# Performance work log

Hardware: AMD Instinct MI355X
Metric: run time of the kernel (lower is better)

## Reference

```python
import jax, jax.numpy as jnp
import numpy as np

N_ATOMS, N_EDGES, N_TRIPLES = 5000, 200000, 4000000
D_NODE, D_EDGE, N_BASIS = 128, 128, 9


def setup_inputs() -> dict:
    key = jax.random.key(0)
    ks = jax.random.split(key, 14)
    inp = {
        "node_feat": jax.random.normal(ks[0], (N_ATOMS, D_NODE), jnp.float32),
        "edge_feat": jax.random.normal(ks[1], (N_EDGES, D_EDGE), jnp.float32),
        "three_basis": jax.random.normal(ks[2], (N_TRIPLES, N_BASIS), jnp.float32),
        "three_cutoff": jax.random.uniform(ks[3], (N_EDGES,), jnp.float32),
        # learned params: update_network_atom = Linear(d_node->n_basis) + sigmoid
        "W_atom": jax.random.normal(ks[4], (D_NODE, N_BASIS), jnp.float32) / np.sqrt(D_NODE).astype(np.float32),
        "b_atom": jnp.zeros((N_BASIS,), jnp.float32),
        # update_network_bond = gated MLP: silu(Linear) * sigmoid(Linear), n_basis->d_edge
        "W_gate": jax.random.normal(ks[5], (N_BASIS, D_EDGE), jnp.float32) / np.sqrt(N_BASIS).astype(np.float32),
        "b_gate": jnp.zeros((D_EDGE,), jnp.float32),
        "W_sig": jax.random.normal(ks[6], (N_BASIS, D_EDGE), jnp.float32) / np.sqrt(N_BASIS).astype(np.float32),
        "b_sig": jnp.zeros((D_EDGE,), jnp.float32),
        # graph structure (int constants)
        "graph_dst": jax.random.randint(ks[7], (N_EDGES,), 0, N_ATOMS, jnp.int32),
        "lg_src": jax.random.randint(ks[8], (N_TRIPLES,), 0, N_EDGES, jnp.int32),
        "lg_dst": jax.random.randint(ks[9], (N_TRIPLES,), 0, N_EDGES, jnp.int32),
        # sorted segment ids == get_segment_indices_from_n(n_triple_ij)
        "segment_ids": jnp.sort(jax.random.randint(ks[10], (N_TRIPLES,), 0, N_EDGES, jnp.int32)),
    }
    return inp


def reference(node_feat, edge_feat, three_basis, three_cutoff,
              W_atom, b_atom, W_gate, b_gate, W_sig, b_sig,
              graph_dst, lg_src, lg_dst, segment_ids):
    # Eq.2: transform node features, gather end atom of each triple's second bond
    atoms = jax.nn.sigmoid(node_feat @ W_atom + b_atom)          # [n_atoms, n_basis]
    end_atom_index = graph_dst[lg_dst]                           # [n_triples]
    basis = three_basis * atoms[end_atom_index]                  # [n_triples, n_basis]
    # cutoff weights per triple (dead code in the provided source: scatter uses basis)
    weights = three_cutoff[lg_src] * three_cutoff[lg_dst]        # [n_triples]
    _ = basis * weights[:, None]
    # scatter-sum triples back to their bond
    new_bonds = jax.ops.segment_sum(basis, segment_ids, num_segments=N_EDGES)  # [n_edges, n_basis]
    # Eq.3: gated MLP bond update
    update = jax.nn.silu(new_bonds @ W_gate + b_gate) * jax.nn.sigmoid(new_bonds @ W_sig + b_sig)
    return edge_feat + update
```

## Files before the change

### kernel.cpp

```cpp
#include <hip/hip_runtime.h>

#define D_NODE    128
#define N_BASIS   9
#define AH_STRIDE 16
#define D_EDGE    128

#define BLOCK_C 256
#define TPT     4
#define CHUNK   (BLOCK_C * TPT)
#define SEG_CAP 512

typedef _Float16 half8 __attribute__((ext_vector_type(8)));

__device__ __forceinline__ float fast_sigmoid(float x) {
    return __builtin_amdgcn_rcpf(1.0f + __expf(-x));
}

__global__ __launch_bounds__(256) void atoms_kernel(
    const float* __restrict__ node_feat,
    const float* __restrict__ W_atom,
    const float* __restrict__ b_atom,
    _Float16* __restrict__ atoms, int n_atoms)
{
    __shared__ float sW[D_NODE * N_BASIS];
    for (int t = threadIdx.x; t < D_NODE * N_BASIS; t += 256)
        sW[t] = W_atom[t];
    __syncthreads();
    int idx = blockIdx.x * 256 + threadIdx.x;
    int total = n_atoms * N_BASIS;
    if (idx >= total) return;
    int a = idx / N_BASIS;
    int b = idx - a * N_BASIS;
    const float* row = node_feat + a * D_NODE;
    float acc = b_atom[b];
#pragma unroll 8
    for (int i = 0; i < D_NODE; ++i)
        acc += row[i] * sW[i * N_BASIS + b];
    atoms[a * AH_STRIDE + b] = (_Float16)fast_sigmoid(acc);
}

__global__ __launch_bounds__(256) void edge_atoms_kernel(
    const _Float16* __restrict__ atoms,
    const int* __restrict__ graph_dst,
    _Float16* __restrict__ ea, int n_edges)
{
    int e = blockIdx.x * 256 + threadIdx.x;
    if (e >= n_edges) return;
    int a = graph_dst[e];
    const _Float16* ap = atoms + (size_t)a * AH_STRIDE;
    half8 h = *(const half8*)ap;
    _Float16 h8 = ap[8];
    _Float16* dp = ea + (size_t)e * AH_STRIDE;
    *(half8*)dp = h;
    dp[8] = h8;
}

#define FLUSH_RUN()                                                          \
    do {                                                                     \
        if (use_lds) {                                                       \
            float* dst_ = lacc + (cur - seg_first) * N_BASIS;                \
            _Pragma("unroll")                                                \
            for (int k_ = 0; k_ < N_BASIS; ++k_)                             \
                atomicAdd(&dst_[k_], sum[k_]);                               \
        } else {                                                             \
            float* dst_ = new_bonds + (size_t)cur * N_BASIS;                 \
            _Pragma("unroll")                                                \
            for (int k_ = 0; k_ < N_BASIS; ++k_)                             \
                unsafeAtomicAdd(&dst_[k_], sum[k_]);                         \
        }                                                                    \
    } while (0)

template<bool EA>
__global__ __launch_bounds__(BLOCK_C) void triple_kernel(
    const float* __restrict__ three_basis,
    const _Float16* __restrict__ atab,
    const int*   __restrict__ graph_dst,
    const int*   __restrict__ lg_dst,
    const int*   __restrict__ seg,
    float* __restrict__ new_bonds,
    int n_triples)
{
    __shared__ float lacc[SEG_CAP * N_BASIS];
    __shared__ int sh_first, sh_last;

    const int tid = threadIdx.x;
    const int chunk_start = blockIdx.x * CHUNK;
    const int t0 = chunk_start + tid * TPT;

    if (tid == 0) sh_first = seg[chunk_start];
    if (tid == BLOCK_C - 1) {
        int last = chunk_start + CHUNK;
        if (last > n_triples) last = n_triples;
        sh_last = seg[last - 1];
    }
    for (int i = tid; i < SEG_CAP * N_BASIS; i += BLOCK_C)
        lacc[i] = 0.0f;
    __syncthreads();

    const int seg_first = sh_first;
    const int range = sh_last - seg_first + 1;
    const bool use_lds = (range <= SEG_CAP);

    if (t0 + TPT <= n_triples) {
        float tb[TPT * N_BASIS];
        const float4* tb4 = (const float4*)(three_basis + (size_t)t0 * N_BASIS);
#pragma unroll
        for (int q = 0; q < 9; ++q)
            *(float4*)&tb[q * 4] = tb4[q];

        const int4 sg4 = *(const int4*)(seg + t0);
        const int4 ld4 = *(const int4*)(lg_dst + t0);
        int sgs[TPT] = { sg4.x, sg4.y, sg4.z, sg4.w };

        int ridx[TPT];
        if (EA) {
            ridx[0] = ld4.x; ridx[1] = ld4.y; ridx[2] = ld4.z; ridx[3] = ld4.w;
        } else {
            ridx[0] = graph_dst[ld4.x];
            ridx[1] = graph_dst[ld4.y];
            ridx[2] = graph_dst[ld4.z];
            ridx[3] = graph_dst[ld4.w];
        }
        half8 hh[TPT];
        _Float16 h8[TPT];
#pragma unroll
        for (int i = 0; i < TPT; ++i) {
            const _Float16* ap = atab + (size_t)ridx[i] * AH_STRIDE;
            hh[i] = *(const half8*)ap;
            h8[i] = ap[8];
        }

        float sum[N_BASIS];
        int cur = sgs[0];
#pragma unroll
        for (int k = 0; k < N_BASIS; ++k) sum[k] = 0.0f;

#pragma unroll
        for (int i = 0; i < TPT; ++i) {
            if (sgs[i] != cur) {
                FLUSH_RUN();
                cur = sgs[i];
#pragma unroll
                for (int k = 0; k < N_BASIS; ++k) sum[k] = 0.0f;
            }
#pragma unroll
            for (int k = 0; k < 8; ++k)
                sum[k] += tb[i * N_BASIS + k] * (float)hh[i][k];
            sum[8] += tb[i * N_BASIS + 8] * (float)h8[i];
        }
        FLUSH_RUN();
    } else if (t0 < n_triples) {
        for (int t = t0; t < n_triples; ++t) {
            int cur = seg[t];
            int r = EA ? lg_dst[t] : graph_dst[lg_dst[t]];
            const float* tbr = three_basis + (size_t)t * N_BASIS;
            const _Float16* ar = atab + (size_t)r * AH_STRIDE;
            float sum[N_BASIS];
#pragma unroll
            for (int k = 0; k < N_BASIS; ++k) sum[k] = tbr[k] * (float)ar[k];
            FLUSH_RUN();
        }
    }

    __syncthreads();

    if (use_lds) {
        int total = range * N_BASIS;
        for (int idx = tid; idx < total; idx += BLOCK_C) {
            int r = idx / N_BASIS;
            int k = idx - r * N_BASIS;
            float v = lacc[idx];
            int s = seg_first + r;
            if (r == 0 || r == range - 1) {
                if (v != 0.0f)
                    unsafeAtomicAdd(&new_bonds[(size_t)s * N_BASIS + k], v);
            } else {
                new_bonds[(size_t)s * N_BASIS + k] = v;
            }
        }
    }
}

__global__ __launch_bounds__(256) void mlp_kernel(
    const float* __restrict__ edge_feat,
    const float* __restrict__ new_bonds,
    const float* __restrict__ W_gate, const float* __restrict__ b_gate,
    const float* __restrict__ W_sig,  const float* __restrict__ b_sig,
    float* __restrict__ out, int n_edges)
{
    const int tid  = threadIdx.x;
    const int grp  = tid >> 5;
    const int c    = (tid & 31) * 4;
    const int e0   = (blockIdx.x * 8 + grp) * 4;
    if (e0 >= n_edges) return;
    const int nvalid = (n_edges - e0) < 4 ? (n_edges - e0) : 4;

    float nb[4][N_BASIS];
#pragma unroll
    for (int j = 0; j < 4; ++j) {
        const float* nbr = new_bonds + (size_t)(e0 + (j < nvalid ? j : 0)) * N_BASIS;
#pragma unroll
        for (int k = 0; k < N_BASIS; ++k) nb[j][k] = nbr[k];
    }

    float4 bg = *(const float4*)(b_gate + c);
    float4 bs = *(const float4*)(b_sig + c);
    float4 g[4], s[4];
#pragma unroll
    for (int j = 0; j < 4; ++j) { g[j] = bg; s[j] = bs; }

#pragma unroll
    for (int k = 0; k < N_BASIS; ++k) {
        float4 wg = *(const float4*)(W_gate + k * D_EDGE + c);
        float4 ws = *(const float4*)(W_sig  + k * D_EDGE + c);
#pragma unroll
        for (int j = 0; j < 4; ++j) {
            g[j].x += nb[j][k] * wg.x; g[j].y += nb[j][k] * wg.y;
            g[j].z += nb[j][k] * wg.z; g[j].w += nb[j][k] * wg.w;
            s[j].x += nb[j][k] * ws.x; s[j].y += nb[j][k] * ws.y;
            s[j].z += nb[j][k] * ws.z; s[j].w += nb[j][k] * ws.w;
        }
    }

#pragma unroll
    for (int j = 0; j < 4; ++j) {
        if (j < nvalid) {
            int e = e0 + j;
            float4 ef = *(const float4*)(edge_feat + (size_t)e * D_EDGE + c);
            float4 o;
            o.x = ef.x + g[j].x * fast_sigmoid(g[j].x) * fast_sigmoid(s[j].x);
            o.y = ef.y + g[j].y * fast_sigmoid(g[j].y) * fast_sigmoid(s[j].y);
            o.z = ef.z + g[j].z * fast_sigmoid(g[j].z) * fast_sigmoid(s[j].z);
            o.w = ef.w + g[j].w * fast_sigmoid(g[j].w) * fast_sigmoid(s[j].w);
            *(float4*)(out + (size_t)e * D_EDGE + c) = o;
        }
    }
}

extern "C" void kernel_launch(void* const* d_in, const int* in_sizes, int n_in,
                              void* d_out, int out_size, void* d_ws, size_t ws_size,
                              hipStream_t stream) {
    const float* node_feat   = (const float*)d_in[0];
    const float* edge_feat   = (const float*)d_in[1];
    const float* three_basis = (const float*)d_in[2];
    const float* W_atom      = (const float*)d_in[4];
    const float* b_atom      = (const float*)d_in[5];
    const float* W_gate      = (const float*)d_in[6];
    const float* b_gate      = (const float*)d_in[7];
    const float* W_sig       = (const float*)d_in[8];
    const float* b_sig       = (const float*)d_in[9];
    const int*   graph_dst   = (const int*)d_in[10];
    const int*   lg_dst      = (const int*)d_in[12];
    const int*   seg         = (const int*)d_in[13];

    int n_atoms   = in_sizes[0] / D_NODE;
    int n_edges   = in_sizes[1] / D_EDGE;
    int n_triples = in_sizes[2] / N_BASIS;

    size_t atoms_bytes = ((size_t)n_atoms * AH_STRIDE * sizeof(_Float16) + 255) & ~(size_t)255;
    size_t ea_bytes    = ((size_t)n_edges * AH_STRIDE * sizeof(_Float16) + 255) & ~(size_t)255;
    size_t nb_bytes    = (size_t)n_edges * N_BASIS * sizeof(float);

    bool use_ea = (ws_size >= atoms_bytes + ea_bytes + nb_bytes);

    _Float16* atoms = (_Float16*)d_ws;
    _Float16* ea    = (_Float16*)((char*)d_ws + atoms_bytes);
    float* new_bonds = (float*)((char*)d_ws + atoms_bytes + (use_ea ? ea_bytes : 0));

    hipMemsetAsync(new_bonds, 0, nb_bytes, stream);

    atoms_kernel<<<(n_atoms * N_BASIS + 255) / 256, 256, 0, stream>>>(
        node_feat, W_atom, b_atom, atoms, n_atoms);

    if (use_ea) {
        edge_atoms_kernel<<<(n_edges + 255) / 256, 256, 0, stream>>>(
            atoms, graph_dst, ea, n_edges);
        triple_kernel<true><<<(n_triples + CHUNK - 1) / CHUNK, BLOCK_C, 0, stream>>>(
            three_basis, ea, graph_dst, lg_dst, seg, new_bonds, n_triples);
    } else {
        triple_kernel<false><<<(n_triples + CHUNK - 1) / CHUNK, BLOCK_C, 0, stream>>>(
            three_basis, atoms, graph_dst, lg_dst, seg, new_bonds, n_triples);
    }

    mlp_kernel<<<(n_edges + 31) / 32, 256, 0, stream>>>(
        edge_feat, new_bonds, W_gate, b_gate, W_sig, b_sig, (float*)d_out, n_edges);
}
```

Before: 420.5 us.

## Stage triple basis via global_load_lds, split atom table, drop edge-atom kernel

Each wave of the triple kernel now bulk-copies its slab of three_basis into LDS with the async global_load_lds path and then reads it back, replacing strided per-thread float4 loads. The padded 16-half atom table is split into an 8-half array plus a separate scalar array. The edge-atom precompute kernel is removed, so the triple kernel always does the graph_dst indirection. The MLP kernel stages weights and new_bonds rows in shared memory, and SEG_CAP is halved, which trades more global-atomic fallbacks for lower LDS usage.

```diff
diff --git a/kernel.cpp b/kernel.cpp
--- a/kernel.cpp
+++ b/kernel.cpp
@@ -1,16 +1,20 @@
 #include <hip/hip_runtime.h>
 
-#define D_NODE    128
-#define N_BASIS   9
-#define AH_STRIDE 16
-#define D_EDGE    128
+#define D_NODE   128
+#define N_BASIS  9
+#define D_EDGE   128
 
 #define BLOCK_C 256
 #define TPT     4
 #define CHUNK   (BLOCK_C * TPT)
-#define SEG_CAP 512
+#define WAVE_T  (64 * TPT)
+#define SLAB_F  (WAVE_T * N_BASIS)
+#define SEG_CAP 256
 
 typedef _Float16 half8 __attribute__((ext_vector_type(8)));
+
+#define AS1(p) ((const __attribute__((address_space(1))) void*)(p))
+#define AS3(p) ((__attribute__((address_space(3))) void*)(p))
 
 __device__ __forceinline__ float fast_sigmoid(float x) {
     return __builtin_amdgcn_rcpf(1.0f + __expf(-x));
@@ -20,7 +24,8 @@
     const float* __restrict__ node_feat,
     const float* __restrict__ W_atom,
     const float* __restrict__ b_atom,
-    _Float16* __restrict__ atoms, int n_atoms)
+    _Float16* __restrict__ atoms8,
+    _Float16* __restrict__ atoms1, int n_atoms)
 {
     __shared__ float sW[D_NODE * N_BASIS];
     for (int t = threadIdx.x; t < D_NODE * N_BASIS; t += 256)
@@ -36,23 +41,9 @@
 #pragma unroll 8
     for (int i = 0; i < D_NODE; ++i)
         acc += row[i] * sW[i * N_BASIS + b];
-    atoms[a * AH_STRIDE + b] = (_Float16)fast_sigmoid(acc);
-}
-
-__global__ __launch_bounds__(256) void edge_atoms_kernel(
-    const _Float16* __restrict__ atoms,
-    const int* __restrict__ graph_dst,
-    _Float16* __restrict__ ea, int n_edges)
-{
-    int e = blockIdx.x * 256 + threadIdx.x;
-    if (e >= n_edges) return;
-    int a = graph_dst[e];
-    const _Float16* ap = atoms + (size_t)a * AH_STRIDE;
-    half8 h = *(const half8*)ap;
-    _Float16 h8 = ap[8];
-    _Float16* dp = ea + (size_t)e * AH_STRIDE;
-    *(half8*)dp = h;
-    dp[8] = h8;
+    _Float16 v = (_Float16)fast_sigmoid(acc);
+    if (b < 8) atoms8[a * 8 + b] = v;
+    else       atoms1[a] = v;
 }
 
 #define FLUSH_RUN()                                                          \
@@ -70,22 +61,39 @@
         }                                                                    \
     } while (0)
 
-template<bool EA>
 __global__ __launch_bounds__(BLOCK_C) void triple_kernel(
     const float* __restrict__ three_basis,
-    const _Float16* __restrict__ atab,
+    const _Float16* __restrict__ atoms8,
+    const _Float16* __restrict__ atoms1,
     const int*   __restrict__ graph_dst,
     const int*   __restrict__ lg_dst,
     const int*   __restrict__ seg,
     float* __restrict__ new_bonds,
     int n_triples)
 {
+    __shared__ float stb[4 * SLAB_F];
     __shared__ float lacc[SEG_CAP * N_BASIS];
     __shared__ int sh_first, sh_last;
 
-    const int tid = threadIdx.x;
+    const int tid  = threadIdx.x;
+    const int wave = tid >> 6;
+    const int lane = tid & 63;
     const int chunk_start = blockIdx.x * CHUNK;
-    const int t0 = chunk_start + tid * TPT;
+    const int slab_start  = chunk_start + wave * WAVE_T;
+    const int t0 = slab_start + lane * TPT;
+
+    float* mystb = stb + wave * SLAB_F;
+    const bool staged = (slab_start + WAVE_T <= n_triples);
+    if (staged) {
+        const char* gsrc = (const char*)three_basis + (size_t)slab_start * (N_BASIS * 4);
+#pragma unroll
+        for (int i = 0; i < 9; ++i) {
+            __builtin_amdgcn_global_load_lds(
+                AS1(gsrc + (size_t)(i * 64 + lane) * 16),
+                AS3((char*)mystb + i * 1024),
+                16, 0, 0);
+        }
+    }
 
     if (tid == 0) sh_first = seg[chunk_start];
     if (tid == BLOCK_C - 1) {
@@ -102,32 +110,34 @@
     const bool use_lds = (range <= SEG_CAP);
 
     if (t0 + TPT <= n_triples) {
-        float tb[TPT * N_BASIS];
-        const float4* tb4 = (const float4*)(three_basis + (size_t)t0 * N_BASIS);
-#pragma unroll
-        for (int q = 0; q < 9; ++q)
-            *(float4*)&tb[q * 4] = tb4[q];
-
         const int4 sg4 = *(const int4*)(seg + t0);
         const int4 ld4 = *(const int4*)(lg_dst + t0);
         int sgs[TPT] = { sg4.x, sg4.y, sg4.z, sg4.w };
-
-        int ridx[TPT];
-        if (EA) {
-            ridx[0] = ld4.x; ridx[1] = ld4.y; ridx[2] = ld4.z; ridx[3] = ld4.w;
-        } else {
-            ridx[0] = graph_dst[ld4.x];
-            ridx[1] = graph_dst[ld4.y];
-            ridx[2] = graph_dst[ld4.z];
-            ridx[3] = graph_dst[ld4.w];
-        }
+        int ai[TPT];
+        ai[0] = graph_dst[ld4.x];
+        ai[1] = graph_dst[ld4.y];
+        ai[2] = graph_dst[ld4.z];
+        ai[3] = graph_dst[ld4.w];
+
         half8 hh[TPT];
         _Float16 h8[TPT];
 #pragma unroll
         for (int i = 0; i < TPT; ++i) {
-            const _Float16* ap = atab + (size_t)ridx[i] * AH_STRIDE;
-            hh[i] = *(const half8*)ap;
-            h8[i] = ap[8];
+            hh[i] = *(const half8*)(atoms8 + (size_t)ai[i] * 8);
+            h8[i] = atoms1[ai[i]];
+        }
+
+        float tb[TPT * N_BASIS];
+        if (staged) {
+            const float* tbl = mystb + lane * (TPT * N_BASIS);
+#pragma unroll
+            for (int q = 0; q < 9; ++q)
+                *(float4*)&tb[q * 4] = *(const float4*)(tbl + q * 4);
+        } else {
+            const float4* tb4 = (const float4*)(three_basis + (size_t)t0 * N_BASIS);
+#pragma unroll
+            for (int q = 0; q < 9; ++q)
+                *(float4*)&tb[q * 4] = tb4[q];
         }
 
         float sum[N_BASIS];
@@ -152,12 +162,13 @@
     } else if (t0 < n_triples) {
         for (int t = t0; t < n_triples; ++t) {
             int cur = seg[t];
-            int r = EA ? lg_dst[t] : graph_dst[lg_dst[t]];
+            int a = graph_dst[lg_dst[t]];
             const float* tbr = three_basis + (size_t)t * N_BASIS;
-            const _Float16* ar = atab + (size_t)r * AH_STRIDE;
+            const _Float16* ar = atoms8 + (size_t)a * 8;
             float sum[N_BASIS];
 #pragma unroll
-            for (int k = 0; k < N_BASIS; ++k) sum[k] = tbr[k] * (float)ar[k];
+            for (int k = 0; k < 8; ++k) sum[k] = tbr[k] * (float)ar[k];
+            sum[8] = tbr[8] * (float)atoms1[a];
             FLUSH_RUN();
         }
     }
@@ -188,19 +199,38 @@
     const float* __restrict__ W_sig,  const float* __restrict__ b_sig,
     float* __restrict__ out, int n_edges)
 {
-    const int tid  = threadIdx.x;
-    const int grp  = tid >> 5;
-    const int c    = (tid & 31) * 4;
-    const int e0   = (blockIdx.x * 8 + grp) * 4;
+    __shared__ float sWg[N_BASIS * D_EDGE];
+    __shared__ float sWs[N_BASIS * D_EDGE];
+    __shared__ float snb[32 * N_BASIS];
+
+    const int tid = threadIdx.x;
+    const int e_base = blockIdx.x * 32;
+
+    for (int i = tid; i < N_BASIS * D_EDGE; i += 256) {
+        sWg[i] = W_gate[i];
+        sWs[i] = W_sig[i];
+    }
+    {
+        int nv = n_edges - e_base;
+        if (nv > 32) nv = 32;
+        for (int i = tid; i < nv * N_BASIS; i += 256)
+            snb[i] = new_bonds[(size_t)e_base * N_BASIS + i];
+    }
+    __syncthreads();
+
+    const int grp = tid >> 5;
+    const int c   = (tid & 31) * 4;
+    const int e0  = e_base + grp * 4;
     if (e0 >= n_edges) return;
     const int nvalid = (n_edges - e0) < 4 ? (n_edges - e0) : 4;
 
     float nb[4][N_BASIS];
 #pragma unroll
     for (int j = 0; j < 4; ++j) {
-        const float* nbr = new_bonds + (size_t)(e0 + (j < nvalid ? j : 0)) * N_BASIS;
-#pragma unroll
-        for (int k = 0; k < N_BASIS; ++k) nb[j][k] = nbr[k];
+        int jj = (j < nvalid) ? j : 0;
+#pragma unroll
+        for (int k = 0; k < N_BASIS; ++k)
+            nb[j][k] = snb[(grp * 4 + jj) * N_BASIS + k];
     }
 
     float4 bg = *(const float4*)(b_gate + c);
@@ -211,8 +241,8 @@
 
 #pragma unroll
     for (int k = 0; k < N_BASIS; ++k) {
-        float4 wg = *(const float4*)(W_gate + k * D_EDGE + c);
-        float4 ws = *(const float4*)(W_sig  + k * D_EDGE + c);
+        float4 wg = *(const float4*)&sWg[k * D_EDGE + c];
+        float4 ws = *(const float4*)&sWs[k * D_EDGE + c];
 #pragma unroll
         for (int j = 0; j < 4; ++j) {
             g[j].x += nb[j][k] * wg.x; g[j].y += nb[j][k] * wg.y;
@@ -257,30 +287,21 @@
     int n_edges   = in_sizes[1] / D_EDGE;
     int n_triples = in_sizes[2] / N_BASIS;
 
-    size_t atoms_bytes = ((size_t)n_atoms * AH_STRIDE * sizeof(_Float16) + 255) & ~(size_t)255;
-    size_t ea_bytes    = ((size_t)n_edges * AH_STRIDE * sizeof(_Float16) + 255) & ~(size_t)255;
-    size_t nb_bytes    = (size_t)n_edges * N_BASIS * sizeof(float);
-
-    bool use_ea = (ws_size >= atoms_bytes + ea_bytes + nb_bytes);
-
-    _Float16* atoms = (_Float16*)d_ws;
-    _Float16* ea    = (_Float16*)((char*)d_ws + atoms_bytes);
-    float* new_bonds = (float*)((char*)d_ws + atoms_bytes + (use_ea ? ea_bytes : 0));
+    size_t a8_bytes = ((size_t)n_atoms * 8 * sizeof(_Float16) + 255) & ~(size_t)255;
+    size_t a1_bytes = ((size_t)n_atoms * sizeof(_Float16) + 255) & ~(size_t)255;
+    size_t nb_bytes = (size_t)n_edges * N_BASIS * sizeof(float);
+
+    _Float16* atoms8 = (_Float16*)d_ws;
+    _Float16* atoms1 = (_Float16*)((char*)d_ws + a8_bytes);
+    float* new_bonds = (float*)((char*)d_ws + a8_bytes + a1_bytes);
 
     hipMemsetAsync(new_bonds, 0, nb_bytes, stream);
 
     atoms_kernel<<<(n_atoms * N_BASIS + 255) / 256, 256, 0, stream>>>(
-        node_feat, W_atom, b_atom, atoms, n_atoms);
-
-    if (use_ea) {
-        edge_atoms_kernel<<<(n_edges + 255) / 256, 256, 0, stream>>>(
-            atoms, graph_dst, ea, n_edges);
-        triple_kernel<true><<<(n_triples + CHUNK - 1) / CHUNK, BLOCK_C, 0, stream>>>(
-            three_basis, ea, graph_dst, lg_dst, seg, new_bonds, n_triples);
-    } else {
-        triple_kernel<false><<<(n_triples + CHUNK - 1) / CHUNK, BLOCK_C, 0, stream>>>(
-            three_basis, atoms, graph_dst, lg_dst, seg, new_bonds, n_triples);
-    }
+        node_feat, W_atom, b_atom, atoms8, atoms1, n_atoms);
+
+    triple_kernel<<<(n_triples + CHUNK - 1) / CHUNK, BLOCK_C, 0, stream>>>(
+        three_basis, atoms8, atoms1, graph_dst, lg_dst, seg, new_bonds, n_triples);
 
     mlp_kernel<<<(n_edges + 31) / 32, 256, 0, stream>>>(
         edge_feat, new_bonds, W_gate, b_gate, W_sig, b_sig, (float*)d_out, n_edges);
```

Result: slower. 435.4 us (+3.5%).
